# Kernel tuning notes

Measured on AMD Instinct MI355X. Metric: run time of the kernel, lower is better.

## Reference

```python
import jax, jax.numpy as jnp
import numpy as np

N, E, B = 50000, 800000, 128
NF, ED, HID, HEADS, DH, OUT, L = 7, 2, 128, 4, 32, 64, 3
EPS = 1e-5
NEG_SLOPE = 0.2


def _layer_norm(x, g, b):
    mu = jnp.mean(x, axis=-1, keepdims=True)
    v = jnp.mean((x - mu) ** 2, axis=-1, keepdims=True)
    return g * (x - mu) / jnp.sqrt(v + EPS) + b


def setup_inputs() -> dict:
    key = jax.random.key(0)
    ks = jax.random.split(key, 32)
    s = 0.05
    inp = {
        "x": jax.random.normal(ks[0], (N, NF), jnp.float32),
        "edge_index": jax.random.randint(ks[1], (2, E), 0, N, jnp.int32),
        "edge_attr": jax.random.uniform(ks[2], (E, ED), jnp.float32),
        "batch": jnp.sort(jax.random.randint(ks[3], (N,), 0, B, jnp.int32)),
        # node encoder
        "enc_W": jax.random.normal(ks[4], (NF, HID)) * (1.0 / np.sqrt(NF)),
        "enc_b": jnp.zeros((HID,)),
        "enc_g": jnp.ones((HID,)),
        "enc_bb": jnp.zeros((HID,)),
        # GATv2 layers (stacked over L)
        "gat_Wsrc": jax.random.normal(ks[5], (L, HID, HID)) * (1.0 / np.sqrt(HID)),
        "gat_Wdst": jax.random.normal(ks[6], (L, HID, HID)) * (1.0 / np.sqrt(HID)),
        "gat_We": jax.random.normal(ks[7], (L, ED, HID)) * (1.0 / np.sqrt(ED)),
        "gat_att": jax.random.normal(ks[8], (L, HEADS, DH)) * s,
        "gat_bias": jnp.zeros((L, HID)),
        # GraphNorm per layer
        "gn_w": jnp.ones((L, HID)),
        "gn_b": jnp.zeros((L, HID)),
        "gn_s": jnp.ones((L, HID)),  # mean_scale
        # attention pooling
        "pool_W1": jax.random.normal(ks[9], (HID, HID)) * (1.0 / np.sqrt(HID)),
        "pool_b1": jnp.zeros((HID,)),
        "pool_W2": jax.random.normal(ks[10], (HID, 1)) * (1.0 / np.sqrt(HID)),
        # output mapper
        "map_W1": jax.random.normal(ks[11], (HID, HID)) * (1.0 / np.sqrt(HID)),
        "map_b1": jnp.zeros((HID,)),
        "map_g": jnp.ones((HID,)),
        "map_bb": jnp.zeros((HID,)),
        "map_W2": jax.random.normal(ks[12], (HID, OUT)) * (1.0 / np.sqrt(HID)),
        "map_b2": jnp.zeros((OUT,)),
    }
    return inp


def _segment_softmax(scores, seg, num_seg):
    # scores: [E2, HEADS], seg: [E2] destination node ids
    m = jax.ops.segment_max(scores, seg, num_segments=num_seg)
    ex = jnp.exp(scores - m[seg])
    denom = jax.ops.segment_sum(ex, seg, num_segments=num_seg)
    return ex / denom[seg]


def _gatv2(x, src, dst, ea, Wsrc, Wdst, We, att, bias):
    e2 = src.shape[0]
    xl = (x @ Wsrc)[src].reshape(e2, HEADS, DH)   # lin_l(x_j), source
    xr = (x @ Wdst)[dst].reshape(e2, HEADS, DH)   # lin_r(x_i), target
    ee = (ea @ We).reshape(e2, HEADS, DH)
    z = jax.nn.leaky_relu(xl + xr + ee, NEG_SLOPE)
    score = jnp.einsum("ehd,hd->eh", z, att)
    alpha = _segment_softmax(score, dst, N)       # softmax over incoming edges
    msg = (xl * alpha[:, :, None]).reshape(e2, HID)
    out = jax.ops.segment_sum(msg, dst, num_segments=N)
    return out + bias


def _graph_norm(x, batch, w, b, scale):
    cnt = jax.ops.segment_sum(jnp.ones((N,), x.dtype), batch, num_segments=B)
    cnt = jnp.maximum(cnt, 1.0)[:, None]
    mean = jax.ops.segment_sum(x, batch, num_segments=B) / cnt
    xc = x - scale * mean[batch]
    var = jax.ops.segment_sum(xc * xc, batch, num_segments=B) / cnt
    return w * xc / jnp.sqrt(var[batch] + EPS) + b


def reference(x, edge_index, edge_attr, batch, enc_W, enc_b, enc_g, enc_bb,
              gat_Wsrc, gat_Wdst, gat_We, gat_att, gat_bias, gn_w, gn_b, gn_s,
              pool_W1, pool_b1, pool_W2, map_W1, map_b1, map_g, map_bb,
              map_W2, map_b2):
    # node encoder: Linear -> ReLU -> LayerNorm
    h = _layer_norm(jax.nn.relu(x @ enc_W + enc_b), enc_g, enc_bb)

    # add self loops; self-loop edge_attr = mean of edge_attr (PyG fill_value='mean')
    loop = jnp.arange(N, dtype=edge_index.dtype)
    src = jnp.concatenate([edge_index[0], loop])
    dst = jnp.concatenate([edge_index[1], loop])
    ea_mean = jnp.mean(edge_attr, axis=0)
    ea = jnp.concatenate([edge_attr, jnp.broadcast_to(ea_mean, (N, ED))], axis=0)

    for i in range(L):
        out = _gatv2(h, src, dst, ea, gat_Wsrc[i], gat_Wdst[i], gat_We[i],
                     gat_att[i], gat_bias[i])
        out = out + h  # residual (in_dim == out_dim -> Identity proj)
        out = _graph_norm(out, batch, gn_w[i], gn_b[i], gn_s[i])
        h = jax.nn.elu(out)

    node_emb = h
    # attention pooling: softmax over ALL nodes (dim=0, as in source)
    scores = jnp.tanh(h @ pool_W1 + pool_b1) @ pool_W2          # [N, 1]
    weights = jax.nn.softmax(scores, axis=0)
    g = jax.ops.segment_sum(h * weights, batch, num_segments=B)  # [B, HID]

    # output mapper (dropout inactive at eval)
    g = _layer_norm(jax.nn.relu(g @ map_W1 + map_b1), map_g, map_bb)
    graph_emb = g @ map_W2 + map_b2
    return graph_emb, node_emb
```

## Files before the change

### kernel.cpp

```cpp
#include <hip/hip_runtime.h>
#include <hip/hip_bf16.h>

typedef __hip_bfloat16 bf16;
typedef __attribute__((ext_vector_type(8))) short short8;
typedef __attribute__((ext_vector_type(4))) float float4v;

#define Nn   50000
#define Ee   800000
#define E2   850000
#define Bb   128
#define NFd  7
#define HID  128
#define OUTD 64
#define EPS  1e-5f
#define SLOPE 0.2f
#define NSTRIP 3125
#define NPAIR  1563

#define MFMA16(a,b,c) __builtin_amdgcn_mfma_f32_16x16x32_bf16(a,b,c,0,0,0)

__device__ __forceinline__ float lane_bcast(float v, int l){
  return __int_as_float(__builtin_amdgcn_readlane(__float_as_int(v), l));
}
__device__ __forceinline__ float wred_sum(float v){
  #pragma unroll
  for (int o=32;o;o>>=1) v += __shfl_xor(v, o, 64);
  return v;
}
__device__ __forceinline__ float gred16_sum(float v){
  v += __shfl_xor(v,1,64); v += __shfl_xor(v,2,64);
  v += __shfl_xor(v,4,64); v += __shfl_xor(v,8,64);
  return v;
}
__device__ __forceinline__ unsigned fkey(float f){
  unsigned u = __float_as_uint(f);
  return (u & 0x80000000u) ? ~u : (u | 0x80000000u);
}
__device__ __forceinline__ float fkeyinv(unsigned k){
  unsigned u = (k & 0x80000000u) ? (k ^ 0x80000000u) : ~k;
  return __uint_as_float(u);
}
__device__ __forceinline__ float tanh_fast(float x){
  float e = __expf(fminf(fmaxf(2.f*x, -30.f), 30.f));
  return (e-1.f)/(e+1.f);
}
__device__ __forceinline__ float bf_lo(unsigned u){ return __uint_as_float(u<<16); }
__device__ __forceinline__ float bf_hi(unsigned u){ return __uint_as_float(u & 0xffff0000u); }
__device__ __forceinline__ unsigned short f2bs(float f){
  bf16 h = __float2bfloat16(f);
  return *reinterpret_cast<unsigned short*>(&h);
}
__device__ __forceinline__ unsigned pack2(float a, float b){
  return (unsigned)f2bs(a) | ((unsigned)f2bs(b) << 16);
}
__device__ __forceinline__ int xcd_swizzle(int bid, int nwg){
  int q = nwg >> 3, r = nwg & 7;
  int x = bid & 7, i = bid >> 3;
  return (x < r ? x*(q+1) : r*(q+1) + (x-r)*q) + i;
}

__global__ __launch_bounds__(256) void k_encoder(
    const float* __restrict__ x, const float* __restrict__ W, const float* __restrict__ b,
    const float* __restrict__ g, const float* __restrict__ bbv,
    float* __restrict__ h, unsigned* __restrict__ hbu){
  int wv = (blockIdx.x*blockDim.x + threadIdx.x) >> 6;
  if (wv >= Nn) return;
  int lane = threadIdx.x & 63;
  int d0 = 2*lane, d1 = d0+1;
  float y0 = b[d0], y1 = b[d1];
  #pragma unroll
  for (int i=0;i<NFd;++i){
    float xv = x[wv*NFd + i];
    y0 = fmaf(xv, W[i*HID + d0], y0);
    y1 = fmaf(xv, W[i*HID + d1], y1);
  }
  y0 = fmaxf(y0, 0.f); y1 = fmaxf(y1, 0.f);
  float mu = wred_sum(y0+y1) * (1.f/HID);
  float c0 = y0-mu, c1 = y1-mu;
  float var = wred_sum(c0*c0 + c1*c1) * (1.f/HID);
  float rs = rsqrtf(var + EPS);
  float v0 = g[d0]*c0*rs + bbv[d0];
  float v1 = g[d1]*c1*rs + bbv[d1];
  *(float2*)(h + (size_t)wv*HID + d0) = make_float2(v0, v1);
  hbu[(size_t)wv*64 + lane] = pack2(v0, v1);
}

__global__ void k_ea_mean(const float* __restrict__ ea, float* __restrict__ eam){
  int tid = blockIdx.x*blockDim.x + threadIdx.x;
  const float2* ea2 = (const float2*)ea;
  float a0=0.f, a1=0.f;
  for (int e=tid; e<Ee; e += gridDim.x*blockDim.x){
    float2 v = ea2[e];
    a0 += v.x; a1 += v.y;
  }
  a0 = wred_sum(a0); a1 = wred_sum(a1);
  if ((threadIdx.x & 63)==0){
    atomicAdd(&eam[0], a0*(1.f/Ee));
    atomicAdd(&eam[1], a1*(1.f/Ee));
  }
}

__global__ void k_deg(const int* __restrict__ ei, int* __restrict__ deg){
  int e = blockIdx.x*blockDim.x + threadIdx.x;
  if (e >= E2) return;
  int d = (e < Ee) ? ei[Ee + e] : (e - Ee);
  atomicAdd(&deg[d], 1);
}

__global__ __launch_bounds__(1024) void k_scan(const int* __restrict__ deg,
    int* __restrict__ offs, int* __restrict__ cursor){
  __shared__ int wsum[16];
  __shared__ int tot_s;
  __shared__ int carry_s;
  int t = threadIdx.x, lane = t & 63, wid = t >> 6;
  if (t==0) carry_s = 0;
  __syncthreads();
  for (int base=0; base<Nn; base += 1024){
    int i = base + t;
    int v = (i < Nn) ? deg[i] : 0;
    int x = v;
    #pragma unroll
    for (int o=1;o<64;o<<=1){ int u = __shfl_up(x, o, 64); if (lane >= o) x += u; }
    if (lane==63) wsum[wid] = x;
    __syncthreads();
    if (t==0){ int s=0; for (int k=0;k<16;++k){ int tv=wsum[k]; wsum[k]=s; s+=tv; } tot_s = s; }
    __syncthreads();
    int excl = carry_s + wsum[wid] + x - v;
    if (i < Nn){ offs[i] = excl; cursor[i] = excl; }
    __syncthreads();
    if (t==0) carry_s += tot_s;
    __syncthreads();
  }
  if (t==0) offs[Nn] = carry_s;
}

__global__ void k_scatter(const int* __restrict__ ei, const float* __restrict__ ea,
    const float* __restrict__ eam, int* __restrict__ cursor,
    int* __restrict__ csrc, float2* __restrict__ cea){
  int e = blockIdx.x*blockDim.x + threadIdx.x;
  if (e >= E2) return;
  int s, d; float a0, a1;
  if (e < Ee){
    s = ei[e]; d = ei[Ee + e];
    float2 v = ((const float2*)ea)[e];
    a0 = v.x; a1 = v.y;
  } else {
    s = d = e - Ee; a0 = eam[0]; a1 = eam[1];
  }
  int pos = atomicAdd(&cursor[d], 1);
  csrc[pos] = s;
  cea[pos] = make_float2(a0, a1);
}

__global__ void k_gstart(const int* __restrict__ batch, int* __restrict__ gstart){
  int n = blockIdx.x*blockDim.x + threadIdx.x;
  if (n >= Nn) return;
  int bc = batch[n];
  int bp = (n==0) ? -1 : batch[n-1];
  for (int b = bp+1; b <= bc; ++b) gstart[b] = n;
  if (n == Nn-1){ for (int b = bc+1; b <= Bb; ++b) gstart[b] = Nn; }
}

__global__ __launch_bounds__(256) void k_dualgemm(
    const unsigned* __restrict__ hbu,
    const float* __restrict__ Wsrc, const float* __restrict__ Wdst,
    unsigned* __restrict__ hsb, float* __restrict__ hd){
  __shared__ unsigned short wt[256*HID];
  #pragma unroll
  for (int iter=0; iter<64; ++iter){
    int idx = iter*256 + threadIdx.x;
    int n = idx & 255, kp = idx >> 8;
    const float* Wp = (n < 128) ? Wsrc : (Wdst - 128);
    float w0 = Wp[(2*kp)*HID + n];
    float w1 = Wp[(2*kp+1)*HID + n];
    int byt = (n*256 + kp*4) ^ ((n&7)<<4);
    *(unsigned*)((char*)wt + byt) = pack2(w0, w1);
  }
  __syncthreads();
  int wid = threadIdx.x >> 6, lane = threadIdx.x & 63;
  int q = lane >> 4, c = lane & 15;
  const unsigned short* hb = (const unsigned short*)hbu;
  for (int pr = blockIdx.x*4 + wid; pr < NPAIR; pr += gridDim.x*4){
    int p0 = 2*pr, p1 = 2*pr + 1;
    bool v1 = (p1 < NSTRIP);
    int node0 = p0*16 + c;
    int node1 = v1 ? (p1*16 + c) : node0;
    short8 bf0[4], bf1[4];
    const unsigned short* hp0 = hb + (size_t)node0*HID + q*8;
    const unsigned short* hp1 = hb + (size_t)node1*HID + q*8;
    #pragma unroll
    for (int s=0;s<4;++s){
      bf0[s] = *(const short8*)(hp0 + s*32);
      bf1[s] = *(const short8*)(hp1 + s*32);
    }
    #pragma unroll 4
    for (int t=0;t<16;++t){
      float4v ac0 = {0.f,0.f,0.f,0.f}, ac1 = {0.f,0.f,0.f,0.f};
      #pragma unroll
      for (int s=0;s<4;++s){
        int row = t*16 + c;
        int byt = (row*256 + s*64 + q*16) ^ ((row&7)<<4);
        short8 af = *(const short8*)((const char*)wt + byt);
        ac0 = MFMA16(af, bf0[s], ac0);
        ac1 = MFMA16(af, bf1[s], ac1);
      }
      if (t < 8){
        int co = t*8 + q*2;
        *(uint2*)(hsb + (size_t)node0*64 + co) =
            make_uint2(pack2(ac0[0],ac0[1]), pack2(ac0[2],ac0[3]));
        if (v1) *(uint2*)(hsb + (size_t)node1*64 + co) =
            make_uint2(pack2(ac1[0],ac1[1]), pack2(ac1[2],ac1[3]));
      } else {
        int dd = (t-8)*16 + q*4;
        *(float4*)(hd + (size_t)node0*HID + dd) = make_float4(ac0[0],ac0[1],ac0[2],ac0[3]);
        if (v1) *(float4*)(hd + (size_t)node1*HID + dd) = make_float4(ac1[0],ac1[1],ac1[2],ac1[3]);
      }
    }
  }
}

__global__ __launch_bounds__(256) void k_edge(const unsigned* __restrict__ hsb,
    float* __restrict__ hdio, const float* __restrict__ h,
    const int* __restrict__ csrc, const float2* __restrict__ cea,
    const int* __restrict__ offs, const float* __restrict__ We,
    const float* __restrict__ att, const float* __restrict__ bias){
  int bid = xcd_swizzle(blockIdx.x, gridDim.x);
  int n = (bid*256 + (int)threadIdx.x) >> 6;
  if (n >= Nn) return;
  int lane = threadIdx.x & 63;
  int d0 = 2*lane, d1 = d0+1;
  float we00 = We[d0],       we01 = We[d1];
  float we10 = We[HID+d0],   we11 = We[HID+d1];
  float at0  = att[(lane>>4)*32 + (d0&31)];
  float at1  = att[(lane>>4)*32 + (d1&31)];
  float2 xr = *(const float2*)(hdio + (size_t)n*HID + d0);
  int e0 = offs[n], e1 = offs[n+1];
  float m = -1e30f, ssum = 0.f, acc0 = 0.f, acc1 = 0.f;

  int e = e0;
  int npair = (e1 - e0) >> 1;
  int sA, sB; float2 eA, eB; unsigned xA, xB;
  if (npair > 0){
    sA = csrc[e]; sB = csrc[e+1];
    eA = cea[e];  eB = cea[e+1];
    xA = hsb[(size_t)sA*64 + lane];
    xB = hsb[(size_t)sB*64 + lane];
  }
  for (int i = 0; i < npair; ++i){
    int sA_n=0, sB_n=0; float2 eA_n, eB_n; unsigned xA_n=0, xB_n=0;
    if (i+1 < npair){
      int en = e + 2;
      sA_n = csrc[en]; sB_n = csrc[en+1];
      eA_n = cea[en];  eB_n = cea[en+1];
      xA_n = hsb[(size_t)sA_n*64 + lane];
      xB_n = hsb[(size_t)sB_n*64 + lane];
    }
    float xA0 = bf_lo(xA), xA1 = bf_hi(xA);
    float xB0 = bf_lo(xB), xB1 = bf_hi(xB);
    float zA0 = fmaf(eA.y, we10, fmaf(eA.x, we00, xA0 + xr.x));
    float zA1 = fmaf(eA.y, we11, fmaf(eA.x, we01, xA1 + xr.y));
    float zB0 = fmaf(eB.y, we10, fmaf(eB.x, we00, xB0 + xr.x));
    float zB1 = fmaf(eB.y, we11, fmaf(eB.x, we01, xB1 + xr.y));
    zA0 = fmaxf(zA0, SLOPE*zA0); zA1 = fmaxf(zA1, SLOPE*zA1);
    zB0 = fmaxf(zB0, SLOPE*zB0); zB1 = fmaxf(zB1, SLOPE*zB1);
    float scA = gred16_sum(fmaf(zA1, at1, zA0*at0));
    float scB = gred16_sum(fmaf(zB1, at1, zB0*at0));
    float mAB = fmaxf(scA, scB);
    float nm = fmaxf(m, mAB);
    float pA = __expf(scA - nm);
    float pB = __expf(scB - nm);
    if (__any(mAB > m)){
      float f = __expf(m - nm);
      ssum = fmaf(ssum, f, pA + pB);
      acc0 = fmaf(acc0, f, fmaf(pA, xA0, pB*xB0));
      acc1 = fmaf(acc1, f, fmaf(pA, xA1, pB*xB1));
      m = nm;
    } else {
      ssum += pA + pB;
      acc0 = fmaf(pB, xB0, fmaf(pA, xA0, acc0));
      acc1 = fmaf(pB, xB1, fmaf(pA, xA1, acc1));
    }
    e += 2;
    sA=sA_n; sB=sB_n; eA=eA_n; eB=eB_n; xA=xA_n; xB=xB_n;
  }
  if (e < e1){
    int s = csrc[e]; float2 eav = cea[e];
    unsigned xu = hsb[(size_t)s*64 + lane];
    float x0 = bf_lo(xu), x1 = bf_hi(xu);
    float z0 = fmaf(eav.y, we10, fmaf(eav.x, we00, x0 + xr.x));
    float z1 = fmaf(eav.y, we11, fmaf(eav.x, we01, x1 + xr.y));
    z0 = fmaxf(z0, SLOPE*z0); z1 = fmaxf(z1, SLOPE*z1);
    float sc = gred16_sum(fmaf(z1, at1, z0*at0));
    float nm = fmaxf(m, sc);
    float p = __expf(sc - nm);
    if (__any(sc > m)){
      float f = __expf(m - nm);
      ssum = fmaf(ssum, f, p);
      acc0 = fmaf(acc0, f, p*x0);
      acc1 = fmaf(acc1, f, p*x1);
    } else {
      ssum += p;
      acc0 = fmaf(p, x0, acc0);
      acc1 = fmaf(p, x1, acc1);
    }
  }
  float inv = 1.f/ssum;
  float o0 = acc0*inv + bias[d0] + h[(size_t)n*HID + d0];
  float o1 = acc1*inv + bias[d1] + h[(size_t)n*HID + d1];
  *(float2*)(hdio + (size_t)n*HID + d0) = make_float2(o0, o1);
}

__global__ __launch_bounds__(128) void k_gn_reduce(const float* __restrict__ out,
    const int* __restrict__ gstart, float* __restrict__ gsum_, float* __restrict__ gsq_){
  int b = blockIdx.x >> 4, sub = blockIdx.x & 15;
  int ns = gstart[b], ne = gstart[b+1];
  int d = threadIdx.x;
  float s = 0.f, qq = 0.f;
  for (int n = ns + sub; n < ne; n += 16){
    float v = out[(size_t)n*HID + d];
    s += v; qq = fmaf(v, v, qq);
  }
  atomicAdd(&gsum_[b*HID + d], s);
  atomicAdd(&gsq_[b*HID + d], qq);
}

__global__ __launch_bounds__(256) void k_gn_apply(const float* __restrict__ out,
    const float* __restrict__ gsum_, const float* __restrict__ gsq_,
    const int* __restrict__ gstart, const int* __restrict__ batch,
    const float* __restrict__ gw, const float* __restrict__ gb,
    const float* __restrict__ gs, float* __restrict__ h,
    unsigned* __restrict__ hbu, float* __restrict__ emb){
  int n = (blockIdx.x*blockDim.x + threadIdx.x) >> 6;
  if (n >= Nn) return;
  int lane = threadIdx.x & 63;
  int b = batch[n];
  float icnt = 1.f / fmaxf((float)(gstart[b+1]-gstart[b]), 1.f);
  int d0 = 2*lane, d1 = d0+1;
  float2 x = *(const float2*)(out + (size_t)n*HID + d0);
  float mean0 = gsum_[b*HID+d0]*icnt, mean1 = gsum_[b*HID+d1]*icnt;
  float ms0 = mean0*gs[d0], ms1 = mean1*gs[d1];
  float var0 = gsq_[b*HID+d0]*icnt - ms0*(2.f*mean0 - ms0);
  float var1 = gsq_[b*HID+d1]*icnt - ms1*(2.f*mean1 - ms1);
  float rs0 = rsqrtf(fmaxf(var0, 0.f) + EPS);
  float rs1 = rsqrtf(fmaxf(var1, 0.f) + EPS);
  float y0 = gw[d0]*(x.x - ms0)*rs0 + gb[d0];
  float y1 = gw[d1]*(x.y - ms1)*rs1 + gb[d1];
  y0 = (y0 > 0.f) ? y0 : (__expf(y0) - 1.f);
  y1 = (y1 > 0.f) ? y1 : (__expf(y1) - 1.f);
  *(float2*)(h + (size_t)n*HID + d0) = make_float2(y0, y1);
  hbu[(size_t)n*64 + lane] = pack2(y0, y1);
  if (emb) *(float2*)(emb + (size_t)n*HID + d0) = make_float2(y0, y1);
}

__global__ __launch_bounds__(256) void k_pool_score(
    const unsigned* __restrict__ hbu,
    const float* __restrict__ W1, const float* __restrict__ b1, const float* __restrict__ W2,
    float* __restrict__ score, unsigned* __restrict__ mkey){
  __shared__ unsigned short wt[HID*HID];
  __shared__ float b1l[HID], w2l[HID];
  #pragma unroll
  for (int iter=0; iter<32; ++iter){
    int idx = iter*256 + threadIdx.x;
    int n = idx & 127, kp = idx >> 7;
    float w0 = W1[(2*kp)*HID + n];
    float w1 = W1[(2*kp+1)*HID + n];
    int byt = (n*256 + kp*4) ^ ((n&7)<<4);
    *(unsigned*)((char*)wt + byt) = pack2(w0, w1);
  }
  if (threadIdx.x < HID){ b1l[threadIdx.x] = b1[threadIdx.x]; w2l[threadIdx.x] = W2[threadIdx.x]; }
  __syncthreads();
  int wid = threadIdx.x >> 6, lane = threadIdx.x & 63;
  int q = lane >> 4, c = lane & 15;
  const unsigned short* hb = (const unsigned short*)hbu;
  float bmax = -1e30f;
  for (int p = blockIdx.x*4 + wid; p < NSTRIP; p += gridDim.x*4){
    int node = p*16 + c;
    short8 bf[4];
    const unsigned short* hp = hb + (size_t)node*HID + q*8;
    #pragma unroll
    for (int s=0;s<4;++s) bf[s] = *(const short8*)(hp + s*32);
    float part = 0.f;
    #pragma unroll
    for (int t=0;t<8;++t){
      float4v ac = {0.f,0.f,0.f,0.f};
      #pragma unroll
      for (int s=0;s<4;++s){
        int row = t*16 + c;
        int byt = (row*256 + s*64 + q*16) ^ ((row&7)<<4);
        ac = MFMA16(*(const short8*)((const char*)wt + byt), bf[s], ac);
      }
      int dim = t*16 + q*4;
      #pragma unroll
      for (int r=0;r<4;++r)
        part += tanh_fast(ac[r] + b1l[dim+r]) * w2l[dim+r];
    }
    part += __shfl_xor(part, 16, 64);
    part += __shfl_xor(part, 32, 64);
    if (q==0) score[node] = part;
    bmax = fmaxf(bmax, part);
  }
  #pragma unroll
  for (int o=32;o;o>>=1) bmax = fmaxf(bmax, __shfl_xor(bmax, o, 64));
  if (lane==0) atomicMax(mkey, fkey(bmax));
}

__global__ __launch_bounds__(128) void k_pool_reduce(const float* __restrict__ h,
    const float* __restrict__ score, const unsigned* __restrict__ mkey,
    const int* __restrict__ gstart, float* __restrict__ gsum, float* __restrict__ total){
  int b = blockIdx.x >> 4, sub = blockIdx.x & 15;
  int ns = gstart[b], ne = gstart[b+1];
  float mx = fkeyinv(*mkey);
  int d = threadIdx.x;
  float acc = 0.f, es = 0.f;
  for (int n = ns + sub; n < ne; n += 16){
    float ev = __expf(score[n] - mx);
    acc = fmaf(ev, h[(size_t)n*HID + d], acc);
    if (d==0) es += ev;
  }
  atomicAdd(&gsum[b*HID + d], acc);
  if (d==0) atomicAdd(total, es);
}

__global__ __launch_bounds__(64) void k_mapper(const float* __restrict__ gsum,
    const float* __restrict__ total,
    const float* __restrict__ W1, const float* __restrict__ b1,
    const float* __restrict__ g,  const float* __restrict__ bbv,
    const float* __restrict__ W2, const float* __restrict__ b2v,
    float* __restrict__ out0){
  int b = blockIdx.x, lane = threadIdx.x;
  float inv = 1.f/(*total);
  int d0 = 2*lane, d1 = d0+1;
  float gv0 = gsum[b*HID + d0]*inv, gv1 = gsum[b*HID + d1]*inv;
  float a0 = b1[d0], a1 = b1[d1];
  for (int i=0;i<HID;++i){
    float hv = lane_bcast((i&1) ? gv1 : gv0, i>>1);
    a0 = fmaf(hv, W1[i*HID + d0], a0);
    a1 = fmaf(hv, W1[i*HID + d1], a1);
  }
  a0 = fmaxf(a0, 0.f); a1 = fmaxf(a1, 0.f);
  float mu = wred_sum(a0+a1) * (1.f/HID);
  float c0 = a0-mu, c1 = a1-mu;
  float var = wred_sum(c0*c0 + c1*c1) * (1.f/HID);
  float rs = rsqrtf(var + EPS);
  float l0 = g[d0]*c0*rs + bbv[d0];
  float l1 = g[d1]*c1*rs + bbv[d1];
  float acc = b2v[lane];
  for (int j=0;j<HID;++j){
    float lv = lane_bcast((j&1) ? l1 : l0, j>>1);
    acc = fmaf(lv, W2[j*OUTD + lane], acc);
  }
  out0[b*OUTD + lane] = acc;
}

extern "C" void kernel_launch(void* const* d_in, const int* in_sizes, int n_in,
                              void* d_out, int out_size, void* d_ws, size_t ws_size,
                              hipStream_t stream){
  const float* x     = (const float*)d_in[0];
  const int*   ei    = (const int*)  d_in[1];
  const float* ea    = (const float*)d_in[2];
  const int*   batch = (const int*)  d_in[3];
  const float* encW  = (const float*)d_in[4];
  const float* encb  = (const float*)d_in[5];
  const float* encg  = (const float*)d_in[6];
  const float* encbb = (const float*)d_in[7];
  const float* gWsrc = (const float*)d_in[8];
  const float* gWdst = (const float*)d_in[9];
  const float* gWe   = (const float*)d_in[10];
  const float* gatt  = (const float*)d_in[11];
  const float* gbias = (const float*)d_in[12];
  const float* gnw   = (const float*)d_in[13];
  const float* gnb   = (const float*)d_in[14];
  const float* gns   = (const float*)d_in[15];
  const float* pW1   = (const float*)d_in[16];
  const float* pb1   = (const float*)d_in[17];
  const float* pW2   = (const float*)d_in[18];
  const float* mW1   = (const float*)d_in[19];
  const float* mb1   = (const float*)d_in[20];
  const float* mg    = (const float*)d_in[21];
  const float* mbb   = (const float*)d_in[22];
  const float* mW2   = (const float*)d_in[23];
  const float* mb2   = (const float*)d_in[24];

  char* w = (char*)d_ws;
  size_t off = 0;
  auto alloc = [&](size_t bytes)->char*{
    char* p = w + off;
    off += (bytes + 255) & ~(size_t)255;
    return p;
  };
  float*    h      = (float*)   alloc((size_t)Nn*HID*4);
  unsigned* hbu    = (unsigned*)alloc((size_t)Nn*64*4);
  unsigned* hsb    = (unsigned*)alloc((size_t)Nn*64*4);
  float*    hd     = (float*)   alloc((size_t)Nn*HID*4);
  int*      csrc   = (int*)     alloc((size_t)E2*4);
  float2*   cea    = (float2*)  alloc((size_t)E2*8);
  int*      offs   = (int*)     alloc((size_t)(Nn+1)*4);
  int*      cursor = (int*)     alloc((size_t)Nn*4);
  int*      deg    = (int*)     alloc((size_t)Nn*4);
  int*      gstart = (int*)     alloc((size_t)(Bb+1)*4);
  float*    score  = (float*)   alloc((size_t)Nn*4);
  float*    gsum   = (float*)   alloc((size_t)Bb*HID*4);
  float*    gnsum  = (float*)   alloc((size_t)Bb*HID*4*2);
  float*    scal   = (float*)   alloc(256);
  float*    eam   = scal;
  float*    total = scal + 2;
  unsigned* mkey  = (unsigned*)(scal + 3);
  float*    gnsq  = gnsum + Bb*HID;

  float* out_graph = (float*)d_out;
  float* out_node  = (float*)d_out + (size_t)Bb*OUTD;

  hipMemsetAsync(deg,  0, (size_t)Nn*4, stream);
  hipMemsetAsync(scal, 0, 256, stream);
  hipMemsetAsync(gsum, 0, (size_t)Bb*HID*4, stream);

  k_encoder<<<Nn/4, 256, 0, stream>>>(x, encW, encb, encg, encbb, h, hbu);
  k_ea_mean<<<256, 256, 0, stream>>>(ea, eam);
  k_deg<<<(E2+255)/256, 256, 0, stream>>>(ei, deg);
  k_scan<<<1, 1024, 0, stream>>>(deg, offs, cursor);
  k_scatter<<<(E2+255)/256, 256, 0, stream>>>(ei, ea, eam, cursor, csrc, cea);
  k_gstart<<<(Nn+255)/256, 256, 0, stream>>>(batch, gstart);

  for (int l = 0; l < 3; ++l){
    k_dualgemm<<<256, 256, 0, stream>>>(hbu, gWsrc + (size_t)l*HID*HID,
                                        gWdst + (size_t)l*HID*HID, hsb, hd);
    k_edge<<<Nn/4, 256, 0, stream>>>(hsb, hd, h, csrc, cea, offs,
                                     gWe + (size_t)l*2*HID,
                                     gatt + (size_t)l*4*32,
                                     gbias + (size_t)l*HID);
    hipMemsetAsync(gnsum, 0, (size_t)Bb*HID*4*2, stream);
    k_gn_reduce<<<Bb*16, 128, 0, stream>>>(hd, gstart, gnsum, gnsq);
    k_gn_apply<<<Nn/4, 256, 0, stream>>>(hd, gnsum, gnsq, gstart, batch,
                                         gnw + (size_t)l*HID, gnb + (size_t)l*HID,
                                         gns + (size_t)l*HID, h, hbu,
                                         (l==2) ? out_node : (float*)nullptr);
  }

  k_pool_score<<<256, 256, 0, stream>>>(hbu, pW1, pb1, pW2, score, mkey);
  k_pool_reduce<<<Bb*16, 128, 0, stream>>>(h, score, mkey, gstart, gsum, total);
  k_mapper<<<Bb, 64, 0, stream>>>(gsum, total, mW1, mb1, mg, mbb, mW2, mb2, out_graph);
}
```

Before: 637.8 us.

## Drop online-max rescaling in edge softmax, use DPP reductions and exp2

```diff
diff --git a/kernel.cpp b/kernel.cpp
--- a/kernel.cpp
+++ b/kernel.cpp
@@ -14,6 +14,7 @@
 #define OUTD 64
 #define EPS  1e-5f
 #define SLOPE 0.2f
+#define LOG2E 1.4426950408889634f
 #define NSTRIP 3125
 #define NPAIR  1563
 
@@ -27,10 +28,15 @@
   for (int o=32;o;o>>=1) v += __shfl_xor(v, o, 64);
   return v;
 }
-__device__ __forceinline__ float gred16_sum(float v){
-  v += __shfl_xor(v,1,64); v += __shfl_xor(v,2,64);
-  v += __shfl_xor(v,4,64); v += __shfl_xor(v,8,64);
-  return v;
+__device__ __forceinline__ float dpp_ror_add(float x, const int ctrl_is_below);
+#define DPP_ROR_ADD(x, ctrl) \
+  ((x) + __int_as_float(__builtin_amdgcn_update_dpp(0, __float_as_int(x), (ctrl), 0xf, 0xf, false)))
+__device__ __forceinline__ float red16_dpp(float x){
+  x = DPP_ROR_ADD(x, 0x121);
+  x = DPP_ROR_ADD(x, 0x122);
+  x = DPP_ROR_ADD(x, 0x124);
+  x = DPP_ROR_ADD(x, 0x128);
+  return x;
 }
 __device__ __forceinline__ unsigned fkey(float f){
   unsigned u = __float_as_uint(f);
@@ -115,18 +121,37 @@
   int t = threadIdx.x, lane = t & 63, wid = t >> 6;
   if (t==0) carry_s = 0;
   __syncthreads();
-  for (int base=0; base<Nn; base += 1024){
-    int i = base + t;
-    int v = (i < Nn) ? deg[i] : 0;
-    int x = v;
+  for (int base=0; base<Nn; base += 4096){
+    int i0 = base + t*4;
+    int v0=0,v1=0,v2=0,v3=0;
+    if (i0+3 < Nn){
+      int4 qv = *(const int4*)(deg + i0);
+      v0=qv.x; v1=qv.y; v2=qv.z; v3=qv.w;
+    } else {
+      if (i0   < Nn) v0 = deg[i0];
+      if (i0+1 < Nn) v1 = deg[i0+1];
+      if (i0+2 < Nn) v2 = deg[i0+2];
+      if (i0+3 < Nn) v3 = deg[i0+3];
+    }
+    int tot = v0+v1+v2+v3;
+    int x = tot;
     #pragma unroll
     for (int o=1;o<64;o<<=1){ int u = __shfl_up(x, o, 64); if (lane >= o) x += u; }
     if (lane==63) wsum[wid] = x;
     __syncthreads();
     if (t==0){ int s=0; for (int k=0;k<16;++k){ int tv=wsum[k]; wsum[k]=s; s+=tv; } tot_s = s; }
     __syncthreads();
-    int excl = carry_s + wsum[wid] + x - v;
-    if (i < Nn){ offs[i] = excl; cursor[i] = excl; }
+    int excl = carry_s + wsum[wid] + (x - tot);
+    int p0 = excl, p1 = excl+v0, p2 = p1+v1, p3 = p2+v2;
+    if (i0+3 < Nn){
+      *(int4*)(offs + i0)   = make_int4(p0,p1,p2,p3);
+      *(int4*)(cursor + i0) = make_int4(p0,p1,p2,p3);
+    } else {
+      if (i0   < Nn){ offs[i0]  =p0; cursor[i0]  =p0; }
+      if (i0+1 < Nn){ offs[i0+1]=p1; cursor[i0+1]=p1; }
+      if (i0+2 < Nn){ offs[i0+2]=p2; cursor[i0+2]=p2; }
+      if (i0+3 < Nn){ offs[i0+3]=p3; cursor[i0+3]=p3; }
+    }
     __syncthreads();
     if (t==0) carry_s += tot_s;
     __syncthreads();
@@ -231,20 +256,29 @@
   int d0 = 2*lane, d1 = d0+1;
   float we00 = We[d0],       we01 = We[d1];
   float we10 = We[HID+d0],   we11 = We[HID+d1];
-  float at0  = att[(lane>>4)*32 + (d0&31)];
-  float at1  = att[(lane>>4)*32 + (d1&31)];
+  float at0  = att[(lane>>4)*32 + (d0&31)] * LOG2E;
+  float at1  = att[(lane>>4)*32 + (d1&31)] * LOG2E;
   float2 xr = *(const float2*)(hdio + (size_t)n*HID + d0);
   int e0 = offs[n], e1 = offs[n+1];
-  float m = -1e30f, ssum = 0.f, acc0 = 0.f, acc1 = 0.f;
-
-  int e = e0;
-  int npair = (e1 - e0) >> 1;
+
+  unsigned xu = hsb[((unsigned)csrc[e0]<<6) + lane];
+  float2 ev = cea[e0];
+  float xl0 = bf_lo(xu), xl1 = bf_hi(xu);
+  float z0 = fmaf(ev.y, we10, fmaf(ev.x, we00, xl0 + xr.x));
+  float z1 = fmaf(ev.y, we11, fmaf(ev.x, we01, xl1 + xr.y));
+  z0 = fmaxf(z0, SLOPE*z0); z1 = fmaxf(z1, SLOPE*z1);
+  float m = red16_dpp(fmaf(z1, at1, z0*at0));
+  float ssum = 1.f, acc0 = xl0, acc1 = xl1;
+
+  int e = e0 + 1;
+  int rem = e1 - e;
+  int npair = rem >> 1;
   int sA, sB; float2 eA, eB; unsigned xA, xB;
   if (npair > 0){
     sA = csrc[e]; sB = csrc[e+1];
     eA = cea[e];  eB = cea[e+1];
-    xA = hsb[(size_t)sA*64 + lane];
-    xB = hsb[(size_t)sB*64 + lane];
+    xA = hsb[((unsigned)sA<<6) + lane];
+    xB = hsb[((unsigned)sB<<6) + lane];
   }
   for (int i = 0; i < npair; ++i){
     int sA_n=0, sB_n=0; float2 eA_n, eB_n; unsigned xA_n=0, xB_n=0;
@@ -252,8 +286,8 @@
       int en = e + 2;
       sA_n = csrc[en]; sB_n = csrc[en+1];
       eA_n = cea[en];  eB_n = cea[en+1];
-      xA_n = hsb[(size_t)sA_n*64 + lane];
-      xB_n = hsb[(size_t)sB_n*64 + lane];
+      xA_n = hsb[((unsigned)sA_n<<6) + lane];
+      xB_n = hsb[((unsigned)sB_n<<6) + lane];
     }
     float xA0 = bf_lo(xA), xA1 = bf_hi(xA);
     float xB0 = bf_lo(xB), xB1 = bf_hi(xB);
@@ -263,46 +297,28 @@
     float zB1 = fmaf(eB.y, we11, fmaf(eB.x, we01, xB1 + xr.y));
     zA0 = fmaxf(zA0, SLOPE*zA0); zA1 = fmaxf(zA1, SLOPE*zA1);
     zB0 = fmaxf(zB0, SLOPE*zB0); zB1 = fmaxf(zB1, SLOPE*zB1);
-    float scA = gred16_sum(fmaf(zA1, at1, zA0*at0));
-    float scB = gred16_sum(fmaf(zB1, at1, zB0*at0));
-    float mAB = fmaxf(scA, scB);
-    float nm = fmaxf(m, mAB);
-    float pA = __expf(scA - nm);
-    float pB = __expf(scB - nm);
-    if (__any(mAB > m)){
-      float f = __expf(m - nm);
-      ssum = fmaf(ssum, f, pA + pB);
-      acc0 = fmaf(acc0, f, fmaf(pA, xA0, pB*xB0));
-      acc1 = fmaf(acc1, f, fmaf(pA, xA1, pB*xB1));
-      m = nm;
-    } else {
-      ssum += pA + pB;
-      acc0 = fmaf(pB, xB0, fmaf(pA, xA0, acc0));
-      acc1 = fmaf(pB, xB1, fmaf(pA, xA1, acc1));
-    }
+    float scA = red16_dpp(fmaf(zA1, at1, zA0*at0));
+    float scB = red16_dpp(fmaf(zB1, at1, zB0*at0));
+    float pA = exp2f(scA - m);
+    float pB = exp2f(scB - m);
+    ssum += pA + pB;
+    acc0 = fmaf(pA, xA0, fmaf(pB, xB0, acc0));
+    acc1 = fmaf(pA, xA1, fmaf(pB, xB1, acc1));
     e += 2;
     sA=sA_n; sB=sB_n; eA=eA_n; eB=eB_n; xA=xA_n; xB=xB_n;
   }
-  if (e < e1){
-    int s = csrc[e]; float2 eav = cea[e];
-    unsigned xu = hsb[(size_t)s*64 + lane];
-    float x0 = bf_lo(xu), x1 = bf_hi(xu);
-    float z0 = fmaf(eav.y, we10, fmaf(eav.x, we00, x0 + xr.x));
-    float z1 = fmaf(eav.y, we11, fmaf(eav.x, we01, x1 + xr.y));
-    z0 = fmaxf(z0, SLOPE*z0); z1 = fmaxf(z1, SLOPE*z1);
-    float sc = gred16_sum(fmaf(z1, at1, z0*at0));
-    float nm = fmaxf(m, sc);
-    float p = __expf(sc - nm);
-    if (__any(sc > m)){
-      float f = __expf(m - nm);
-      ssum = fmaf(ssum, f, p);
-      acc0 = fmaf(acc0, f, p*x0);
-      acc1 = fmaf(acc1, f, p*x1);
-    } else {
-      ssum += p;
-      acc0 = fmaf(p, x0, acc0);
-      acc1 = fmaf(p, x1, acc1);
-    }
+  if (rem & 1){
+    int s = csrc[e1-1]; float2 eav = cea[e1-1];
+    unsigned xt = hsb[((unsigned)s<<6) + lane];
+    float x0 = bf_lo(xt), x1 = bf_hi(xt);
+    float t0 = fmaf(eav.y, we10, fmaf(eav.x, we00, x0 + xr.x));
+    float t1 = fmaf(eav.y, we11, fmaf(eav.x, we01, x1 + xr.y));
+    t0 = fmaxf(t0, SLOPE*t0); t1 = fmaxf(t1, SLOPE*t1);
+    float sc = red16_dpp(fmaf(t1, at1, t0*at0));
+    float p = exp2f(sc - m);
+    ssum += p;
+    acc0 = fmaf(p, x0, acc0);
+    acc1 = fmaf(p, x1, acc1);
   }
   float inv = 1.f/ssum;
   float o0 = acc0*inv + bias[d0] + h[(size_t)n*HID + d0];
```

Result: faster. 580.0 us (-9.1%).
